# Optimization experiments

Measured on AMD Instinct MI355X. Metric: run time of the kernel, lower is better.

The kernel has to match this reference:

```python
import jax, jax.numpy as jnp
import numpy as np

N_BITS = 8
N_GROUPS = 1
COCO = 0.1
# Calibrated constants: the torch module brute-force searches constraint in {0,.2,...,4}
# and threshold in {off, off+.2, ...} with off=(2**(n+1)-1)/(2**n-2) at init time.
# We model the calibrated (inited=False) steady-state forward with the default-style
# picks constraint=0.8 (the module-level `constraint` global) and threshold=off+1.0.
CONSTRAINT = 0.8
THRESHOLD = 1.0 + (2 ** (N_BITS + 1) - 1) / (2 ** N_BITS - 2)


def setup_inputs() -> dict:
    key = jax.random.key(0)
    x = jax.random.normal(key, (32, 2048, 768), dtype=jnp.float32)
    return {"x": x}


def _forward(x):
    B, T, C = x.shape
    # global calibration statistics (recomputed from x, as __init__ branch does)
    std = jnp.std(x, ddof=1)                      # torch .std() uses ddof=1
    coeff = std / (jnp.max(x) - jnp.min(x))
    mean = jnp.median(x)

    # per-token channel range; token 0 is forced to sort first (scaled by 1e8)
    error_ulg = jnp.max(x, axis=2) - jnp.min(x, axis=2)        # (B, T)
    error_ulg = error_ulg.at[:, 0].multiply(1e8)

    # fraction-of-channels-within-band statistic per token
    band = error_ulg[:, :, None] * coeff * CONSTRAINT           # (B, T, 1)
    attn_std = (jnp.sum(x < mean + band, axis=2)
                - jnp.sum(x < mean - band, axis=2)).astype(x.dtype)  # (B, T)
    attn_std = jnp.clip(attn_std, COCO * C, None)               # constraint > 0 branch
    inv = 1.0 / attn_std
    attn_std = jnp.where(inv > 1.0, 0.0, inv)

    # sort tokens by range, pair largest vs smallest
    inc_idx = jnp.argsort(error_ulg, axis=1)                    # (B, T)
    attn_sort_inc = jnp.take_along_axis(error_ulg, inc_idx, axis=1)
    dec_idx = jnp.flip(inc_idx, axis=1)
    attn_sort_dec = jnp.flip(attn_sort_inc, axis=1)
    score = (attn_sort_dec * jnp.take_along_axis(attn_std, dec_idx, axis=1)
             - attn_sort_inc * jnp.take_along_axis(attn_std, inc_idx, axis=1) * THRESHOLD) / std

    # first index where score < 0, per row (torch nonzero/unique_consecutive trick)
    min_indices = jnp.argmax(score < 0, axis=1)                 # (B,)
    min_indices = jnp.where(jnp.sum(jnp.abs(attn_std)) == 0,
                            jnp.zeros_like(min_indices), min_indices)
    diff = jnp.clip(min_indices - 1, 0, None)[:, None]          # (B, 1)

    # rank of each token when sorted by descending range
    rank = jnp.argsort(jnp.argsort(-error_ulg, axis=1), axis=1)  # (B, T)

    # per-token bit width: top-diff tokens -> n_bits+1, bottom-diff -> n_bits-1
    bits = jnp.where(rank > T - 2 - diff, N_BITS - 1,
                     jnp.where(rank <= diff, N_BITS + 1, N_BITS)).astype(x.dtype)
    n_levels = (2.0 ** bits)[:, None, :, None, None]            # (B,1,T,1,1)

    # per-token min-max scale at base bit width (init_quantization_scale)
    x5 = x.reshape(B, 1, T, N_GROUPS, C // N_GROUPS)
    x_min = jnp.min(x5, axis=-1, keepdims=True)
    x_max = jnp.max(x5, axis=-1, keepdims=True)
    delta = jnp.maximum((x_max - x_min) / (2 ** N_BITS - 1), 1e-8)
    zero_point = jnp.round(-x_min / delta)

    x_int = jnp.round(x5 / delta) + zero_point
    x_quant = jnp.clip(x_int / (n_levels - 1.0), 0.0, 1.0) * (n_levels - 1.0)
    x_dequant = (x_quant - zero_point) * delta
    return x_dequant.reshape(B, T, C)


def reference(x):
    return _forward(x)
```

## Files before the change

### kernel.cpp

```cpp
#include <hip/hip_runtime.h>
#include <stdint.h>
#include <math.h>

#define BB 32
#define TT 2048
#define CC 768
#define NTOK (BB*TT)
#define NTOT 50331648LL
#define RANK0 25165823LL
#define RANK1 25165824LL
#define CTH 0.0009765625f
#define NBLK 2048
#define CSTRIDE 64
#define GCAP 4096

typedef float nf4 __attribute__((ext_vector_type(4)));

__device__ inline unsigned int f2key(float f) {
    unsigned int u = __float_as_uint(f);
    return (u & 0x80000000u) ? ~u : (u | 0x80000000u);
}
__device__ inline float key2f(unsigned int k) {
    unsigned int u = (k & 0x80000000u) ? (k ^ 0x80000000u) : ~k;
    return __uint_as_float(u);
}

template<int NB>
__device__ void sel256(const unsigned int* __restrict__ hist,
                       unsigned long long k, unsigned int* res)
{
    const int t = threadIdx.x;
    constexpr int PER = NB / 256;
    unsigned int loc[PER];
    unsigned long long lsum = 0;
    #pragma unroll
    for (int i = 0; i < PER; ++i) { loc[i] = hist[t * PER + i]; lsum += loc[i]; }
    __shared__ unsigned long long pscan[256];
    pscan[t] = lsum;
    __syncthreads();
    #pragma unroll
    for (int off = 1; off < 256; off <<= 1) {
        unsigned long long v = (t >= off) ? pscan[t - off] : 0ULL;
        __syncthreads();
        pscan[t] += v;
        __syncthreads();
    }
    unsigned long long excl = (t == 0) ? 0ULL : pscan[t - 1];
    if (k >= excl && k < pscan[t]) {
        unsigned long long c = excl;
        #pragma unroll
        for (int i = 0; i < PER; ++i) {
            if (k < c + loc[i]) { res[0] = (unsigned int)(t * PER + i); res[1] = (unsigned int)c; break; }
            c += loc[i];
        }
    }
    __syncthreads();
}

template<int NB>
__device__ void sel1024(const unsigned int* __restrict__ hist,
                        unsigned long long k, unsigned int* res,
                        unsigned long long* pscan)
{
    const int t = threadIdx.x;
    constexpr int PER = NB / 1024;
    unsigned int loc[PER];
    unsigned long long lsum = 0;
    #pragma unroll
    for (int i = 0; i < PER; ++i) { loc[i] = hist[t * PER + i]; lsum += loc[i]; }
    pscan[t] = lsum;
    __syncthreads();
    for (int off = 1; off < 1024; off <<= 1) {
        unsigned long long v = (t >= off) ? pscan[t - off] : 0ULL;
        __syncthreads();
        pscan[t] += v;
        __syncthreads();
    }
    unsigned long long excl = (t == 0) ? 0ULL : pscan[t - 1];
    if (k >= excl && k < pscan[t]) {
        unsigned long long c = excl;
        #pragma unroll
        for (int i = 0; i < PER; ++i) {
            if (k < c + loc[i]) { res[0] = (unsigned int)(t * PER + i); res[1] = (unsigned int)c; break; }
            c += loc[i];
        }
    }
    __syncthreads();
}

__device__ inline void do_finstats(const unsigned int* scal, const double* g_sum,
                                   float* fscal)
{
    float v0 = key2f(scal[8]), v1 = key2f(scal[9]);
    float mean = __fmul_rn(__fadd_rn(v0, v1), 0.5f);
    double s = g_sum[0], ss = g_sum[1];
    const double NN = (double)NTOT;
    double var = (ss - s * s / NN) / (NN - 1.0);
    if (var < 0.0) var = 0.0;
    float stdf = (float)sqrt(var);
    float rng = __fsub_rn(fscal[4], fscal[3]);
    float coeff = __fdiv_rn(stdf, rng);
    fscal[0] = mean; fscal[1] = stdf; fscal[2] = coeff;
}

__global__ __launch_bounds__(256) void k_token_stats(
    const float4* __restrict__ x4, float* __restrict__ tokmin,
    float* __restrict__ tokmax, float* __restrict__ eulg,
    double* __restrict__ pS, double* __restrict__ pSS,
    float* __restrict__ pMn, float* __restrict__ pMx,
    unsigned int* __restrict__ pcnt, unsigned int* __restrict__ pnlt,
    unsigned int* __restrict__ cbuf, unsigned int* __restrict__ hist1,
    unsigned int* __restrict__ scal)
{
    __shared__ unsigned int lbuf[CSTRIDE];
    __shared__ unsigned int lhist[2048];
    __shared__ unsigned int lcnt;
    __shared__ double wS[4], wSS[4];
    __shared__ float wMn[4], wMx[4];
    __shared__ unsigned int wNlt[4];
    for (int i = threadIdx.x; i < 2048; i += 256) lhist[i] = 0;
    if (threadIdx.x == 0) lcnt = 0;
    __syncthreads();
    const int wave = threadIdx.x >> 6, lane = threadIdx.x & 63;

    double aS0 = 0.0, aS1 = 0.0, aS2 = 0.0, aS3 = 0.0;
    double aQ0 = 0.0, aQ1 = 0.0, aQ2 = 0.0, aQ3 = 0.0;
    float gmn = INFINITY, gmx = -INFINITY;
    unsigned int nlt = 0;

    for (int token = blockIdx.x * 4 + wave; token < NTOK; token += gridDim.x * 4) {
        const float4* xp = x4 + (size_t)token * 192;
        float4 v0 = xp[lane];
        float4 v1 = xp[lane + 64];
        float4 v2 = xp[lane + 128];

        float mnx = fminf(fminf(v0.x, v1.x), v2.x);
        float mny = fminf(fminf(v0.y, v1.y), v2.y);
        float mnz = fminf(fminf(v0.z, v1.z), v2.z);
        float mnw = fminf(fminf(v0.w, v1.w), v2.w);
        float mxx = fmaxf(fmaxf(v0.x, v1.x), v2.x);
        float mxy = fmaxf(fmaxf(v0.y, v1.y), v2.y);
        float mxz = fmaxf(fmaxf(v0.z, v1.z), v2.z);
        float mxw = fmaxf(fmaxf(v0.w, v1.w), v2.w);
        float mn = fminf(fminf(mnx, mny), fminf(mnz, mnw));
        float mx = fmaxf(fmaxf(mxx, mxy), fmaxf(mxz, mxw));

        #pragma unroll
        for (int k = 0; k < 3; ++k) {
            float4 v = (k == 0) ? v0 : (k == 1) ? v1 : v2;
            double dx = (double)v.x, dy = (double)v.y, dz = (double)v.z, dw = (double)v.w;
            aS0 += dx; aS1 += dy; aS2 += dz; aS3 += dw;
            aQ0 = fma(dx, dx, aQ0); aQ1 = fma(dy, dy, aQ1);
            aQ2 = fma(dz, dz, aQ2); aQ3 = fma(dw, dw, aQ3);
            nlt += (v.x < -CTH) + (v.y < -CTH) + (v.z < -CTH) + (v.w < -CTH);
            #pragma unroll
            for (int c = 0; c < 4; ++c) {
                float vv = (c == 0) ? v.x : (c == 1) ? v.y : (c == 2) ? v.z : v.w;
                if (vv < CTH && vv >= -CTH) {
                    unsigned int p = atomicAdd(&lcnt, 1u);
                    if (p < CSTRIDE) {
                        unsigned int key = f2key(vv);
                        lbuf[p] = key;
                        atomicAdd(&lhist[key >> 21], 1u);
                    }
                }
            }
        }
        gmn = fminf(gmn, mn); gmx = fmaxf(gmx, mx);
        #pragma unroll
        for (int d = 1; d < 64; d <<= 1) {
            mn = fminf(mn, __shfl_xor(mn, d));
            mx = fmaxf(mx, __shfl_xor(mx, d));
        }
        if (lane == 0) {
            tokmin[token] = mn; tokmax[token] = mx;
            float e = __fsub_rn(mx, mn);
            if ((token & (TT - 1)) == 0) e = __fmul_rn(e, 1e8f);
            eulg[token] = e;
        }
    }
    double accS = (aS0 + aS1) + (aS2 + aS3);
    double accSS = (aQ0 + aQ1) + (aQ2 + aQ3);
    #pragma unroll
    for (int d = 1; d < 64; d <<= 1) {
        accS  += __shfl_xor(accS, d);
        accSS += __shfl_xor(accSS, d);
        gmn = fminf(gmn, __shfl_xor(gmn, d));
        gmx = fmaxf(gmx, __shfl_xor(gmx, d));
        nlt += __shfl_xor(nlt, d);
    }
    if (lane == 0) { wS[wave] = accS; wSS[wave] = accSS; wMn[wave] = gmn;
                     wMx[wave] = gmx; wNlt[wave] = nlt; }
    __syncthreads();
    if (threadIdx.x == 0) {
        pS[blockIdx.x]  = wS[0] + wS[1] + wS[2] + wS[3];
        pSS[blockIdx.x] = wSS[0] + wSS[1] + wSS[2] + wSS[3];
        pMn[blockIdx.x] = fminf(fminf(wMn[0], wMn[1]), fminf(wMn[2], wMn[3]));
        pMx[blockIdx.x] = fmaxf(fmaxf(wMx[0], wMx[1]), fmaxf(wMx[2], wMx[3]));
        pnlt[blockIdx.x] = wNlt[0] + wNlt[1] + wNlt[2] + wNlt[3];
        unsigned int n = lcnt;
        if (n > CSTRIDE) { scal[10] = 1; n = CSTRIDE; }
        pcnt[blockIdx.x] = n;
        lcnt = n;
    }
    __syncthreads();
    {
        unsigned int n = lcnt;
        for (unsigned int i = threadIdx.x; i < n; i += 256)
            cbuf[blockIdx.x * CSTRIDE + i] = lbuf[i];
        for (int i = threadIdx.x; i < 2048; i += 256) {
            unsigned int c = lhist[i];
            if (c) atomicAdd(&hist1[i], c);
        }
    }
}

__global__ __launch_bounds__(1024) void k_scalars_a(
    const double* __restrict__ pS, const double* __restrict__ pSS,
    const float* __restrict__ pMn, const float* __restrict__ pMx,
    const unsigned int* __restrict__ pnlt, const unsigned int* __restrict__ hist1,
    unsigned int* __restrict__ scal, double* __restrict__ g_sum,
    float* __restrict__ fscal)
{
    __shared__ double a[1024], b[1024];
    __shared__ float c[1024], d[1024];
    __shared__ unsigned int f[1024];
    __shared__ unsigned long long pscan[1024];
    __shared__ unsigned int sres[2];
    __shared__ long long srr[2];
    __shared__ unsigned int sflag;
    const int t = threadIdx.x;

    a[t] = pS[t] + pS[t + 1024];
    b[t] = pSS[t] + pSS[t + 1024];
    c[t] = fminf(pMn[t], pMn[t + 1024]);
    d[t] = fmaxf(pMx[t], pMx[t + 1024]);
    f[t] = pnlt[t] + pnlt[t + 1024];
    __syncthreads();
    for (int st = 512; st > 0; st >>= 1) {
        if (t < st) {
            a[t] += a[t + st]; b[t] += b[t + st];
            c[t] = fminf(c[t], c[t + st]); d[t] = fmaxf(d[t], d[t + st]);
            f[t] += f[t + st];
        }
        __syncthreads();
    }
    if (t == 0) {
        g_sum[0] = a[0]; g_sum[1] = b[0]; fscal[3] = c[0]; fscal[4] = d[0];
        long long nlt = (long long)f[0];
        srr[0] = RANK0 - nlt; srr[1] = RANK1 - nlt;
        sflag = scal[10];
        if (srr[0] < 0 || srr[1] < 0) sflag = 1;
    }
    __syncthreads();

    for (int r = 0; r < 2; ++r) {
        unsigned long long rin = (srr[r] < 0) ? ~0ULL : (unsigned long long)srr[r];
        sel1024<2048>(hist1, rin, sres, pscan);
        unsigned long long total = pscan[1023];
        if (t == 0) {
            if (rin >= total) sflag = 1;
            else { scal[2 + r] = sres[0]; scal[4 + r] = (unsigned int)(rin - sres[1]); }
        }
        __syncthreads();
    }
    if (t == 0) scal[10] = sflag;
}

__global__ __launch_bounds__(256) void k_gather(
    const unsigned int* __restrict__ cbuf, const unsigned int* __restrict__ pcnt,
    const unsigned int* __restrict__ scal, unsigned int* __restrict__ gcnt,
    unsigned int* __restrict__ gbuf0, unsigned int* __restrict__ gbuf1)
{
    if (scal[10]) return;
    const unsigned int b0 = scal[2], b1 = scal[3];
    const unsigned int nslots = NBLK * CSTRIDE;
    for (unsigned int i = blockIdx.x * 256 + threadIdx.x; i < nslots;
         i += gridDim.x * 256) {
        if ((i & (CSTRIDE - 1)) < pcnt[i >> 6]) {
            unsigned int k = cbuf[i];
            unsigned int bkt = k >> 21;
            if (bkt == b0) {
                unsigned int p = atomicAdd(&gcnt[0], 1u);
                if (p < GCAP) gbuf0[p] = k;
            }
            if (bkt == b1 && b1 != b0) {
                unsigned int p = atomicAdd(&gcnt[1], 1u);
                if (p < GCAP) gbuf1[p] = k;
            }
        }
    }
}

__global__ __launch_bounds__(256) void k_median_final(
    unsigned int* __restrict__ scal, const unsigned int* __restrict__ gcnt,
    const unsigned int* __restrict__ gbuf0, const unsigned int* __restrict__ gbuf1,
    const double* __restrict__ g_sum, float* __restrict__ fscal)
{
    __shared__ unsigned int karr[GCAP];
    __shared__ unsigned int hist[2048];
    __shared__ unsigned int sres[2];
    __shared__ unsigned int sflag;
    const int t = threadIdx.x;
    if (t == 0) {
        unsigned int fl = scal[10];
        if (gcnt[0] > GCAP || gcnt[1] > GCAP) fl = 1;
        scal[10] = fl; sflag = fl;
    }
    __syncthreads();
    if (sflag) return;

    const unsigned int b0 = scal[2], b1 = scal[3];
    for (int r = 0; r < 2; ++r) {
        const bool use0 = (r == 0) || (b1 == b0);
        const unsigned int* gb = use0 ? gbuf0 : gbuf1;
        const unsigned int m = use0 ? gcnt[0] : gcnt[1];
        unsigned long long rin = scal[4 + r];
        for (unsigned int i = t; i < m; i += 256) karr[i] = gb[i];
        for (int i = t; i < 2048; i += 256) hist[i] = 0;
        __syncthreads();
        for (unsigned int i = t; i < m; i += 256)
            atomicAdd(&hist[(karr[i] >> 10) & 2047u], 1u);
        __syncthreads();
        sel256<2048>(hist, rin, sres);
        unsigned int b2 = sres[0]; rin -= sres[1];
        __syncthreads();
        for (int i = t; i < 1024; i += 256) hist[i] = 0;
        __syncthreads();
        for (unsigned int i = t; i < m; i += 256) {
            unsigned int k = karr[i];
            if (((k >> 10) & 2047u) == b2) atomicAdd(&hist[k & 1023u], 1u);
        }
        __syncthreads();
        sel256<1024>(hist, rin, sres);
        if (t == 0) {
            unsigned int bkt = r ? b1 : b0;
            scal[8 + r] = (bkt << 21) | (b2 << 10) | sres[0];
        }
        __syncthreads();
    }
    if (t == 0) do_finstats(scal, g_sum, fscal);
}

__global__ __launch_bounds__(1024) void k_fallback(const float4* __restrict__ x4,
    unsigned int* __restrict__ scal, const double* __restrict__ g_sum,
    float* __restrict__ fscal)
{
    if (!scal[10]) return;
    __shared__ unsigned int h[2][2048];
    __shared__ unsigned long long pscan[1024];
    __shared__ unsigned int sres[2];
    __shared__ unsigned int sb1[2], sb2[2];
    __shared__ unsigned long long srank[2];
    const int t = threadIdx.x;
    const long long n4 = NTOT / 4;
    for (int i = t; i < 2048; i += 1024) h[0][i] = 0;
    __syncthreads();
    for (long long i = t; i < n4; i += 1024) {
        float4 v = x4[i];
        atomicAdd(&h[0][f2key(v.x) >> 21], 1u);
        atomicAdd(&h[0][f2key(v.y) >> 21], 1u);
        atomicAdd(&h[0][f2key(v.z) >> 21], 1u);
        atomicAdd(&h[0][f2key(v.w) >> 21], 1u);
    }
    __syncthreads();
    for (int r = 0; r < 2; ++r) {
        sel1024<2048>(h[0], r ? RANK1 : RANK0, sres, pscan);
        if (t == 0) { sb1[r] = sres[0]; srank[r] = (r ? RANK1 : RANK0) - sres[1]; }
        __syncthreads();
    }
    for (int i = t; i < 4096; i += 1024) ((unsigned int*)h)[i] = 0;
    __syncthreads();
    for (long long i = t; i < n4; i += 1024) {
        float4 v = x4[i];
        #pragma unroll
        for (int cc = 0; cc < 4; ++cc) {
            float fv = (cc == 0) ? v.x : (cc == 1) ? v.y : (cc == 2) ? v.z : v.w;
            unsigned int k = f2key(fv);
            unsigned int top = k >> 21, mid = (k >> 10) & 2047u;
            if (top == sb1[0]) atomicAdd(&h[0][mid], 1u);
            if (top == sb1[1]) atomicAdd(&h[1][mid], 1u);
        }
    }
    __syncthreads();
    for (int r = 0; r < 2; ++r) {
        sel1024<2048>(h[r], srank[r], sres, pscan);
        if (t == 0) { sb2[r] = sres[0]; srank[r] -= sres[1]; }
        __syncthreads();
    }
    for (int i = t; i < 4096; i += 1024) ((unsigned int*)h)[i] = 0;
    __syncthreads();
    for (long long i = t; i < n4; i += 1024) {
        float4 v = x4[i];
        #pragma unroll
        for (int cc = 0; cc < 4; ++cc) {
            float fv = (cc == 0) ? v.x : (cc == 1) ? v.y : (cc == 2) ? v.z : v.w;
            unsigned int k = f2key(fv);
            unsigned int t22 = k >> 10, low = k & 1023u;
            if (t22 == ((sb1[0] << 11) | sb2[0])) atomicAdd(&h[0][low], 1u);
            if (t22 == ((sb1[1] << 11) | sb2[1])) atomicAdd(&h[1][low], 1u);
        }
    }
    __syncthreads();
    for (int r = 0; r < 2; ++r) {
        sel1024<1024>(h[r], srank[r], sres, pscan);
        if (t == 0) scal[8 + r] = (sb1[r] << 21) | (sb2[r] << 10) | sres[0];
        __syncthreads();
    }
    if (t == 0) do_finstats(scal, g_sum, fscal);
}

__global__ __launch_bounds__(256) void k_count(const float4* __restrict__ x4,
    const float* __restrict__ eulg, const float* __restrict__ fscal, float* __restrict__ attn)
{
    const int wave = threadIdx.x >> 6, lane = threadIdx.x & 63;
    const float mean = fscal[0], coeff = fscal[2];
    for (int token = blockIdx.x * 4 + wave; token < NTOK; token += gridDim.x * 4) {
        float band = __fmul_rn(__fmul_rn(eulg[token], coeff), 0.8f);
        float hi = __fadd_rn(mean, band);
        float lo = __fsub_rn(mean, band);
        const float4* xp = x4 + (size_t)token * 192;
        int d = 0;
        #pragma unroll
        for (int k = 0; k < 3; ++k) {
            float4 v = xp[lane + k * 64];
            d += (v.x < hi) - (v.x < lo) + (v.y < hi) - (v.y < lo)
               + (v.z < hi) - (v.z < lo) + (v.w < hi) - (v.w < lo);
        }
        #pragma unroll
        for (int s = 1; s < 64; s <<= 1) d += __shfl_xor(d, s);
        if (lane == 0) {
            float a = fmaxf((float)d, 76.8f);
            float inv = __fdiv_rn(1.0f, a);
            attn[token] = (inv > 1.0f) ? 0.0f : inv;
        }
    }
}

__device__ inline void bitonic_sort(unsigned long long* keys, int tid, int nthr) {
    for (int k = 2; k <= TT; k <<= 1) {
        for (int j = k >> 1; j > 0; j >>= 1) {
            __syncthreads();
            for (int i = tid; i < TT; i += nthr) {
                int l = i ^ j;
                if (l > i) {
                    unsigned long long a = keys[i], c = keys[l];
                    bool up = ((i & k) == 0);
                    if (up ? (a > c) : (a < c)) { keys[i] = c; keys[l] = a; }
                }
            }
        }
    }
    __syncthreads();
}

__global__ __launch_bounds__(1024) void k_sort(const float* __restrict__ eulg,
    const float* __restrict__ attn, const float* __restrict__ fscal,
    unsigned int* __restrict__ nlev)
{
    int bb = blockIdx.x, tid = threadIdx.x;
    __shared__ unsigned long long keys[TT];
    __shared__ float av[TT];
    __shared__ int firstNeg;
    __shared__ int s_diff;
    const float stdf = fscal[1];
    const float THR = (float)(1.0 + 511.0 / 254.0);

    for (int t = tid; t < TT; t += 1024) {
        float v = eulg[bb * TT + t];
        keys[t] = ((unsigned long long)f2key(v) << 32) | (unsigned int)t;
    }
    if (tid == 0) firstNeg = TT;
    __syncthreads();
    bitonic_sort(keys, tid, 1024);

    for (int t = tid; t < TT; t += 1024)
        av[t] = attn[bb * TT + (unsigned int)(keys[t] & 0xffffffffu)];
    __syncthreads();

    for (int i = tid; i < TT; i += 1024) {
        float vi = key2f((unsigned int)(keys[i] >> 32));
        float vd = key2f((unsigned int)(keys[TT - 1 - i] >> 32));
        float a  = __fmul_rn(vd, av[TT - 1 - i]);
        float bt = __fmul_rn(__fmul_rn(vi, av[i]), THR);
        float sc = __fdiv_rn(__fsub_rn(a, bt), stdf);
        if (sc < 0.0f) atomicMin(&firstNeg, i);
    }
    __syncthreads();
    if (tid == 0) {
        int mi = (firstNeg >= TT) ? 0 : firstNeg;
        s_diff = (mi - 1 > 0) ? (mi - 1) : 0;
    }
    __syncthreads();
    int diffv = s_diff;

    for (int i = tid; i < TT; i += 1024) {
        unsigned long long key = keys[i];
        unsigned int ku = (unsigned int)(key >> 32);
        unsigned long long tlo = ((unsigned long long)ku) << 32;
        int a = 0;
        for (int st = 1024; st > 0; st >>= 1) {
            int c = a + st;
            if (c <= TT && keys[c - 1] < tlo) a = c;
        }
        int b1;
        if (ku == 0xFFFFFFFFu) b1 = TT;
        else {
            unsigned long long thi = ((unsigned long long)(ku + 1)) << 32;
            b1 = 0;
            for (int st = 1024; st > 0; st >>= 1) {
                int c = b1 + st;
                if (c <= TT && keys[c - 1] < thi) b1 = c;
            }
        }
        int rank = TT - b1 + i - a;
        unsigned int token = (unsigned int)(key & 0xffffffffu);
        unsigned int levels = (rank > TT - 2 - diffv) ? 128u
                            : ((rank <= diffv) ? 512u : 256u);
        nlev[bb * TT + token] = levels;
    }
}

__global__ __launch_bounds__(256) void k_quant(const float4* __restrict__ x4,
    const float* __restrict__ tokmin, const float* __restrict__ tokmax,
    const unsigned int* __restrict__ nlev, float4* __restrict__ out)
{
    const int wave = threadIdx.x >> 6, lane = threadIdx.x & 63;
    for (int token = blockIdx.x * 4 + wave; token < NTOK; token += gridDim.x * 4) {
        float mn = tokmin[token], mx = tokmax[token];
        float delta = fmaxf(__fdiv_rn(__fsub_rn(mx, mn), 255.0f), 1e-8f);
        float zp = rintf(__fdiv_rn(-mn, delta));
        float nlm1 = (float)(nlev[token] - 1u);
        const float4* xp = x4 + (size_t)token * 192;
        nf4* op = (nf4*)(out + (size_t)token * 192);
        #pragma unroll
        for (int k = 0; k < 3; ++k) {
            float4 v = xp[lane + k * 64];
            nf4 r;
            #pragma unroll
            for (int c = 0; c < 4; ++c) {
                float vv = (c == 0) ? v.x : (c == 1) ? v.y : (c == 2) ? v.z : v.w;
                float xi = __fadd_rn(rintf(__fdiv_rn(vv, delta)), zp);
                float t = __fdiv_rn(xi, nlm1);
                t = fminf(fmaxf(t, 0.0f), 1.0f);
                float xq = __fmul_rn(t, nlm1);
                r[c] = __fmul_rn(__fsub_rn(xq, zp), delta);
            }
            __builtin_nontemporal_store(r, &op[lane + k * 64]);
        }
    }
}

extern "C" void kernel_launch(void* const* d_in, const int* in_sizes, int n_in,
                              void* d_out, int out_size, void* d_ws, size_t ws_size,
                              hipStream_t stream)
{
    (void)in_sizes; (void)n_in; (void)out_size; (void)ws_size;
    const float* x = (const float*)d_in[0];
    float* out = (float*)d_out;
    char* ws = (char*)d_ws;

    double* g_sum = (double*)ws;
    unsigned int* scal = (unsigned int*)(ws + 16);
    unsigned int* gcnt = (unsigned int*)(ws + 64);
    float* fscal = (float*)(ws + 96);
    unsigned int* hist1 = (unsigned int*)(ws + 128);
    float* tokmin = (float*)(ws + 16384);
    float* tokmax = tokmin + NTOK;
    float* eulg   = tokmax + NTOK;
    float* attn   = eulg + NTOK;
    unsigned int* nlev = (unsigned int*)(attn + NTOK);
    double* pS  = (double*)(ws + 1327104);
    double* pSS = pS + 2048;
    float* pMn  = (float*)(pSS + 2048);
    float* pMx  = pMn + 2048;
    unsigned int* pcnt = (unsigned int*)(ws + 1376256);
    unsigned int* pnlt = (unsigned int*)(ws + 1384448);
    unsigned int* cbuf = (unsigned int*)(ws + 1392640);
    unsigned int* gbuf0 = (unsigned int*)(ws + 1916928);
    unsigned int* gbuf1 = (unsigned int*)(ws + 1933312);

    (void)hipMemsetAsync(ws, 0, 8320, stream);

    k_token_stats<<<NBLK, 256, 0, stream>>>((const float4*)x, tokmin, tokmax, eulg,
                                            pS, pSS, pMn, pMx, pcnt, pnlt, cbuf,
                                            hist1, scal);
    k_scalars_a<<<1, 1024, 0, stream>>>(pS, pSS, pMn, pMx, pnlt, hist1,
                                        scal, g_sum, fscal);
    k_gather<<<128, 256, 0, stream>>>(cbuf, pcnt, scal, gcnt, gbuf0, gbuf1);
    k_median_final<<<1, 256, 0, stream>>>(scal, gcnt, gbuf0, gbuf1, g_sum, fscal);
    k_fallback<<<1, 1024, 0, stream>>>((const float4*)x, scal, g_sum, fscal);
    k_count<<<NBLK, 256, 0, stream>>>((const float4*)x, eulg, fscal, attn);
    k_sort<<<BB, 1024, 0, stream>>>(eulg, attn, fscal, nlev);
    k_quant<<<NBLK, 256, 0, stream>>>((const float4*)x, tokmin, tokmax, nlev, (float4*)out);
}
```

Baseline: 213.7 us.

## Precompute 8-bit quantized codes in stats pass; merge median-selection kernels

The token-stats pass now computes each element's integer quantization code and stores it packed as bytes. The final quantize kernel therefore reads a quarter of the bytes instead of re-reading the float input, and no longer does the per-element divide and round. Rare codes that overflow 8 bits are logged to a list and recomputed from the original input by a small fixup kernel. Separately, the gather and median-final kernels are folded into a single scalar kernel with shuffle reductions, which removes two launches. The costs are extra writes and atomics in the stats pass and a new fixup launch; if more than the list capacity of elements overflow, results could be wrong.

```diff
diff --git a/kernel.cpp b/kernel.cpp
--- a/kernel.cpp
+++ b/kernel.cpp
@@ -12,7 +12,8 @@
 #define CTH 0.0009765625f
 #define NBLK 2048
 #define CSTRIDE 64
-#define GCAP 4096
+#define KCAP 4096
+#define ECAP 1024
 
 typedef float nf4 __attribute__((ext_vector_type(4)));
 
@@ -23,38 +24,6 @@
 __device__ inline float key2f(unsigned int k) {
     unsigned int u = (k & 0x80000000u) ? (k ^ 0x80000000u) : ~k;
     return __uint_as_float(u);
-}
-
-template<int NB>
-__device__ void sel256(const unsigned int* __restrict__ hist,
-                       unsigned long long k, unsigned int* res)
-{
-    const int t = threadIdx.x;
-    constexpr int PER = NB / 256;
-    unsigned int loc[PER];
-    unsigned long long lsum = 0;
-    #pragma unroll
-    for (int i = 0; i < PER; ++i) { loc[i] = hist[t * PER + i]; lsum += loc[i]; }
-    __shared__ unsigned long long pscan[256];
-    pscan[t] = lsum;
-    __syncthreads();
-    #pragma unroll
-    for (int off = 1; off < 256; off <<= 1) {
-        unsigned long long v = (t >= off) ? pscan[t - off] : 0ULL;
-        __syncthreads();
-        pscan[t] += v;
-        __syncthreads();
-    }
-    unsigned long long excl = (t == 0) ? 0ULL : pscan[t - 1];
-    if (k >= excl && k < pscan[t]) {
-        unsigned long long c = excl;
-        #pragma unroll
-        for (int i = 0; i < PER; ++i) {
-            if (k < c + loc[i]) { res[0] = (unsigned int)(t * PER + i); res[1] = (unsigned int)c; break; }
-            c += loc[i];
-        }
-    }
-    __syncthreads();
 }
 
 template<int NB>
@@ -110,7 +79,8 @@
     float* __restrict__ pMn, float* __restrict__ pMx,
     unsigned int* __restrict__ pcnt, unsigned int* __restrict__ pnlt,
     unsigned int* __restrict__ cbuf, unsigned int* __restrict__ hist1,
-    unsigned int* __restrict__ scal)
+    unsigned int* __restrict__ scal, unsigned int* __restrict__ xint,
+    unsigned int* __restrict__ ecnt, unsigned int* __restrict__ elist)
 {
     __shared__ unsigned int lbuf[CSTRIDE];
     __shared__ unsigned int lhist[2048];
@@ -178,6 +148,25 @@
             if ((token & (TT - 1)) == 0) e = __fmul_rn(e, 1e8f);
             eulg[token] = e;
         }
+        float delta = fmaxf(__fdiv_rn(__fsub_rn(mx, mn), 255.0f), 1e-8f);
+        float zp = rintf(__fdiv_rn(-mn, delta));
+        #pragma unroll
+        for (int k = 0; k < 3; ++k) {
+            float4 v = (k == 0) ? v0 : (k == 1) ? v1 : v2;
+            unsigned int pack = 0;
+            #pragma unroll
+            for (int c = 0; c < 4; ++c) {
+                float vv = (c == 0) ? v.x : (c == 1) ? v.y : (c == 2) ? v.z : v.w;
+                float xi = __fadd_rn(rintf(__fdiv_rn(vv, delta)), zp);
+                if (xi >= 256.0f) {
+                    unsigned int e = atomicAdd(ecnt, 1u);
+                    if (e < ECAP) elist[e] = (unsigned int)token * CC + k * 256 + lane * 4 + c;
+                    xi = 255.0f;
+                }
+                pack |= ((unsigned int)xi) << (8 * c);
+            }
+            xint[(size_t)token * 192 + k * 64 + lane] = pack;
+        }
     }
     double accS = (aS0 + aS1) + (aS2 + aS3);
     double accSS = (aQ0 + aQ1) + (aQ2 + aQ3);
@@ -215,131 +204,112 @@
     }
 }
 
-__global__ __launch_bounds__(1024) void k_scalars_a(
+__global__ __launch_bounds__(1024) void k_scalars(
     const double* __restrict__ pS, const double* __restrict__ pSS,
     const float* __restrict__ pMn, const float* __restrict__ pMx,
     const unsigned int* __restrict__ pnlt, const unsigned int* __restrict__ hist1,
+    const unsigned int* __restrict__ pcnt, const unsigned int* __restrict__ cbuf,
     unsigned int* __restrict__ scal, double* __restrict__ g_sum,
     float* __restrict__ fscal)
 {
-    __shared__ double a[1024], b[1024];
-    __shared__ float c[1024], d[1024];
-    __shared__ unsigned int f[1024];
+    __shared__ unsigned short spc[2048];
+    __shared__ unsigned int hist[2048];
     __shared__ unsigned long long pscan[1024];
     __shared__ unsigned int sres[2];
+    __shared__ unsigned int karr[2][KCAP];
+    __shared__ unsigned int kcnt[2];
+    __shared__ double wredS[16], wredQ[16];
+    __shared__ float wredMn[16], wredMx[16];
+    __shared__ unsigned int wredN[16];
     __shared__ long long srr[2];
+    __shared__ unsigned int sbkt[2], srnk[2];
     __shared__ unsigned int sflag;
-    const int t = threadIdx.x;
-
-    a[t] = pS[t] + pS[t + 1024];
-    b[t] = pSS[t] + pSS[t + 1024];
-    c[t] = fminf(pMn[t], pMn[t + 1024]);
-    d[t] = fmaxf(pMx[t], pMx[t + 1024]);
-    f[t] = pnlt[t] + pnlt[t + 1024];
-    __syncthreads();
-    for (int st = 512; st > 0; st >>= 1) {
-        if (t < st) {
-            a[t] += a[t + st]; b[t] += b[t + st];
-            c[t] = fminf(c[t], c[t + st]); d[t] = fmaxf(d[t], d[t + st]);
-            f[t] += f[t + st];
-        }
-        __syncthreads();
-    }
+    const int t = threadIdx.x, wid = t >> 6, lane = t & 63;
+
+    double a = pS[t] + pS[t + 1024];
+    double b = pSS[t] + pSS[t + 1024];
+    float  c = fminf(pMn[t], pMn[t + 1024]);
+    float  d = fmaxf(pMx[t], pMx[t + 1024]);
+    unsigned int f = pnlt[t] + pnlt[t + 1024];
+    #pragma unroll
+    for (int s = 1; s < 64; s <<= 1) {
+        a += __shfl_xor(a, s); b += __shfl_xor(b, s);
+        c = fminf(c, __shfl_xor(c, s)); d = fmaxf(d, __shfl_xor(d, s));
+        f += __shfl_xor(f, s);
+    }
+    if (lane == 0) { wredS[wid] = a; wredQ[wid] = b; wredMn[wid] = c;
+                     wredMx[wid] = d; wredN[wid] = f; }
+    spc[t] = (unsigned short)pcnt[t];
+    spc[t + 1024] = (unsigned short)pcnt[t + 1024];
+    __syncthreads();
     if (t == 0) {
-        g_sum[0] = a[0]; g_sum[1] = b[0]; fscal[3] = c[0]; fscal[4] = d[0];
-        long long nlt = (long long)f[0];
+        double A = 0, B = 0; float C = INFINITY, D = -INFINITY;
+        unsigned long long F = 0;
+        for (int i = 0; i < 16; ++i) {
+            A += wredS[i]; B += wredQ[i];
+            C = fminf(C, wredMn[i]); D = fmaxf(D, wredMx[i]);
+            F += wredN[i];
+        }
+        g_sum[0] = A; g_sum[1] = B; fscal[3] = C; fscal[4] = D;
+        long long nlt = (long long)F;
         srr[0] = RANK0 - nlt; srr[1] = RANK1 - nlt;
-        sflag = scal[10];
-        if (srr[0] < 0 || srr[1] < 0) sflag = 1;
+        unsigned int fl = scal[10];
+        if (srr[0] < 0 || srr[1] < 0) fl = 1;
+        sflag = fl;
+        kcnt[0] = 0; kcnt[1] = 0;
     }
     __syncthreads();
 
     for (int r = 0; r < 2; ++r) {
-        unsigned long long rin = (srr[r] < 0) ? ~0ULL : (unsigned long long)srr[r];
+        unsigned long long rin = (srr[r] < 0) ? 0ULL : (unsigned long long)srr[r];
         sel1024<2048>(hist1, rin, sres, pscan);
-        unsigned long long total = pscan[1023];
         if (t == 0) {
-            if (rin >= total) sflag = 1;
-            else { scal[2 + r] = sres[0]; scal[4 + r] = (unsigned int)(rin - sres[1]); }
-        }
-        __syncthreads();
-    }
-    if (t == 0) scal[10] = sflag;
-}
-
-__global__ __launch_bounds__(256) void k_gather(
-    const unsigned int* __restrict__ cbuf, const unsigned int* __restrict__ pcnt,
-    const unsigned int* __restrict__ scal, unsigned int* __restrict__ gcnt,
-    unsigned int* __restrict__ gbuf0, unsigned int* __restrict__ gbuf1)
-{
-    if (scal[10]) return;
-    const unsigned int b0 = scal[2], b1 = scal[3];
-    const unsigned int nslots = NBLK * CSTRIDE;
-    for (unsigned int i = blockIdx.x * 256 + threadIdx.x; i < nslots;
-         i += gridDim.x * 256) {
-        if ((i & (CSTRIDE - 1)) < pcnt[i >> 6]) {
+            unsigned long long total = pscan[1023];
+            if (srr[r] < 0 || rin >= total) sflag = 1;
+            else { sbkt[r] = sres[0]; srnk[r] = (unsigned int)(rin - sres[1]); }
+        }
+        __syncthreads();
+    }
+    if (sflag) { if (t == 0) scal[10] = 1; return; }
+
+    const unsigned int b0 = sbkt[0], b1 = sbkt[1];
+    for (unsigned int i = t; i < NBLK * CSTRIDE; i += 1024) {
+        if ((i & (CSTRIDE - 1)) < spc[i >> 6]) {
             unsigned int k = cbuf[i];
             unsigned int bkt = k >> 21;
-            if (bkt == b0) {
-                unsigned int p = atomicAdd(&gcnt[0], 1u);
-                if (p < GCAP) gbuf0[p] = k;
-            }
-            if (bkt == b1 && b1 != b0) {
-                unsigned int p = atomicAdd(&gcnt[1], 1u);
-                if (p < GCAP) gbuf1[p] = k;
-            }
-        }
-    }
-}
-
-__global__ __launch_bounds__(256) void k_median_final(
-    unsigned int* __restrict__ scal, const unsigned int* __restrict__ gcnt,
-    const unsigned int* __restrict__ gbuf0, const unsigned int* __restrict__ gbuf1,
-    const double* __restrict__ g_sum, float* __restrict__ fscal)
-{
-    __shared__ unsigned int karr[GCAP];
-    __shared__ unsigned int hist[2048];
-    __shared__ unsigned int sres[2];
-    __shared__ unsigned int sflag;
-    const int t = threadIdx.x;
-    if (t == 0) {
-        unsigned int fl = scal[10];
-        if (gcnt[0] > GCAP || gcnt[1] > GCAP) fl = 1;
-        scal[10] = fl; sflag = fl;
-    }
-    __syncthreads();
-    if (sflag) return;
-
-    const unsigned int b0 = scal[2], b1 = scal[3];
+            if (bkt == b0) { unsigned int p = atomicAdd(&kcnt[0], 1u); if (p < KCAP) karr[0][p] = k; }
+            else if (bkt == b1) { unsigned int p = atomicAdd(&kcnt[1], 1u); if (p < KCAP) karr[1][p] = k; }
+        }
+    }
+    __syncthreads();
+    if (t == 0 && (kcnt[0] > KCAP || kcnt[1] > KCAP)) sflag = 1;
+    __syncthreads();
+    if (sflag) { if (t == 0) scal[10] = 1; return; }
+
     for (int r = 0; r < 2; ++r) {
-        const bool use0 = (r == 0) || (b1 == b0);
-        const unsigned int* gb = use0 ? gbuf0 : gbuf1;
-        const unsigned int m = use0 ? gcnt[0] : gcnt[1];
-        unsigned long long rin = scal[4 + r];
-        for (unsigned int i = t; i < m; i += 256) karr[i] = gb[i];
-        for (int i = t; i < 2048; i += 256) hist[i] = 0;
-        __syncthreads();
-        for (unsigned int i = t; i < m; i += 256)
-            atomicAdd(&hist[(karr[i] >> 10) & 2047u], 1u);
-        __syncthreads();
-        sel256<2048>(hist, rin, sres);
+        int use = (r == 1 && b1 != b0) ? 1 : 0;
+        const unsigned int m = kcnt[use];
+        unsigned long long rin = srnk[r];
+        for (int i = t; i < 2048; i += 1024) hist[i] = 0;
+        __syncthreads();
+        for (unsigned int i = t; i < m; i += 1024)
+            atomicAdd(&hist[(karr[use][i] >> 10) & 2047u], 1u);
+        __syncthreads();
+        sel1024<2048>(hist, rin, sres, pscan);
         unsigned int b2 = sres[0]; rin -= sres[1];
         __syncthreads();
-        for (int i = t; i < 1024; i += 256) hist[i] = 0;
-        __syncthreads();
-        for (unsigned int i = t; i < m; i += 256) {
-            unsigned int k = karr[i];
+        for (int i = t; i < 1024; i += 1024) hist[i] = 0;
+        __syncthreads();
+        for (unsigned int i = t; i < m; i += 1024) {
+            unsigned int k = karr[use][i];
             if (((k >> 10) & 2047u) == b2) atomicAdd(&hist[k & 1023u], 1u);
         }
         __syncthreads();
-        sel256<1024>(hist, rin, sres);
-        if (t == 0) {
-            unsigned int bkt = r ? b1 : b0;
-            scal[8 + r] = (bkt << 21) | (b2 << 10) | sres[0];
-        }
-        __syncthreads();
-    }
-    if (t == 0) do_finstats(scal, g_sum, fscal);
+        sel1024<1024>(hist, rin, sres, pscan);
+        if (t == 0) scal[8 + r] = ((r ? b1 : b0) << 21) | (b2 << 10) | sres[0];
+        __syncthreads();
+    }
+    if (t == 0) { scal[10] = 0; do_finstats(scal, g_sum, fscal); }
 }
 
 __global__ __launch_bounds__(1024) void k_fallback(const float4* __restrict__ x4,
@@ -521,7 +491,7 @@
     }
 }
 
-__global__ __launch_bounds__(256) void k_quant(const float4* __restrict__ x4,
+__global__ __launch_bounds__(256) void k_quant(const unsigned int* __restrict__ xint,
     const float* __restrict__ tokmin, const float* __restrict__ tokmax,
     const unsigned int* __restrict__ nlev, float4* __restrict__ out)
 {
@@ -531,16 +501,15 @@
         float delta = fmaxf(__fdiv_rn(__fsub_rn(mx, mn), 255.0f), 1e-8f);
         float zp = rintf(__fdiv_rn(-mn, delta));
         float nlm1 = (float)(nlev[token] - 1u);
-        const float4* xp = x4 + (size_t)token * 192;
+        const unsigned int* ip = xint + (size_t)token * 192;
         nf4* op = (nf4*)(out + (size_t)token * 192);
         #pragma unroll
         for (int k = 0; k < 3; ++k) {
-            float4 v = xp[lane + k * 64];
+            unsigned int u = ip[lane + k * 64];
             nf4 r;
             #pragma unroll
             for (int c = 0; c < 4; ++c) {
-                float vv = (c == 0) ? v.x : (c == 1) ? v.y : (c == 2) ? v.z : v.w;
-                float xi = __fadd_rn(rintf(__fdiv_rn(vv, delta)), zp);
+                float xi = (float)((u >> (8 * c)) & 0xffu);
                 float t = __fdiv_rn(xi, nlm1);
                 t = fminf(fmaxf(t, 0.0f), 1.0f);
                 float xq = __fmul_rn(t, nlm1);
@@ -551,6 +520,28 @@
     }
 }
 
+__global__ void k_fixup(const float* __restrict__ x, const float* __restrict__ tokmin,
+    const float* __restrict__ tokmax, const unsigned int* __restrict__ nlev,
+    const unsigned int* __restrict__ ecnt, const unsigned int* __restrict__ elist,
+    float* __restrict__ out)
+{
+    unsigned int n = min(ecnt[0], (unsigned int)ECAP);
+    for (unsigned int i = threadIdx.x; i < n; i += 64) {
+        unsigned int idx = elist[i];
+        unsigned int token = idx / CC;
+        float mn = tokmin[token], mx = tokmax[token];
+        float delta = fmaxf(__fdiv_rn(__fsub_rn(mx, mn), 255.0f), 1e-8f);
+        float zp = rintf(__fdiv_rn(-mn, delta));
+        float nlm1 = (float)(nlev[token] - 1u);
+        float vv = x[idx];
+        float xi = __fadd_rn(rintf(__fdiv_rn(vv, delta)), zp);
+        float t = __fdiv_rn(xi, nlm1);
+        t = fminf(fmaxf(t, 0.0f), 1.0f);
+        float xq = __fmul_rn(t, nlm1);
+        out[idx] = __fmul_rn(__fsub_rn(xq, zp), delta);
+    }
+}
+
 extern "C" void kernel_launch(void* const* d_in, const int* in_sizes, int n_in,
                               void* d_out, int out_size, void* d_ws, size_t ws_size,
                               hipStream_t stream)
@@ -562,9 +553,10 @@
 
     double* g_sum = (double*)ws;
     unsigned int* scal = (unsigned int*)(ws + 16);
-    unsigned int* gcnt = (unsigned int*)(ws + 64);
+    unsigned int* ecnt = (unsigned int*)(ws + 64);
     float* fscal = (float*)(ws + 96);
     unsigned int* hist1 = (unsigned int*)(ws + 128);
+    unsigned int* elist = (unsigned int*)(ws + 8320);
     float* tokmin = (float*)(ws + 16384);
     float* tokmax = tokmin + NTOK;
     float* eulg   = tokmax + NTOK;
@@ -577,20 +569,18 @@
     unsigned int* pcnt = (unsigned int*)(ws + 1376256);
     unsigned int* pnlt = (unsigned int*)(ws + 1384448);
     unsigned int* cbuf = (unsigned int*)(ws + 1392640);
-    unsigned int* gbuf0 = (unsigned int*)(ws + 1916928);
-    unsigned int* gbuf1 = (unsigned int*)(ws + 1933312);
+    unsigned int* xint = (unsigned int*)(ws + 2097152);
 
     (void)hipMemsetAsync(ws, 0, 8320, stream);
 
     k_token_stats<<<NBLK, 256, 0, stream>>>((const float4*)x, tokmin, tokmax, eulg,
                                             pS, pSS, pMn, pMx, pcnt, pnlt, cbuf,
-                                            hist1, scal);
-    k_scalars_a<<<1, 1024, 0, stream>>>(pS, pSS, pMn, pMx, pnlt, hist1,
-                                        scal, g_sum, fscal);
-    k_gather<<<128, 256, 0, stream>>>(cbuf, pcnt, scal, gcnt, gbuf0, gbuf1);
-    k_median_final<<<1, 256, 0, stream>>>(scal, gcnt, gbuf0, gbuf1, g_sum, fscal);
+                                            hist1, scal, xint, ecnt, elist);
+    k_scalars<<<1, 1024, 0, stream>>>(pS, pSS, pMn, pMx, pnlt, hist1, pcnt, cbuf,
+                                      scal, g_sum, fscal);
     k_fallback<<<1, 1024, 0, stream>>>((const float4*)x, scal, g_sum, fscal);
     k_count<<<NBLK, 256, 0, stream>>>((const float4*)x, eulg, fscal, attn);
     k_sort<<<BB, 1024, 0, stream>>>(eulg, attn, fscal, nlev);
-    k_quant<<<NBLK, 256, 0, stream>>>((const float4*)x, tokmin, tokmax, nlev, (float4*)out);
-}
+    k_quant<<<NBLK, 256, 0, stream>>>(xint, tokmin, tokmax, nlev, (float4*)out);
+    k_fixup<<<1, 64, 0, stream>>>(x, tokmin, tokmax, nlev, ecnt, elist, out);
+}
```

New measurement: 239.3 us. +12.0%, slower.
